# Kernel tuning notes

Measured on AMD Instinct MI355X. Metric: run time of the kernel, lower is better.

Reference implementation:

```python
import jax, jax.numpy as jnp
import numpy as np
from itertools import product

_N = 50000
_G = 52  # voxel grid extent


def _build_maps():
    rs = np.random.RandomState(0)
    ids = rs.choice(_G ** 3, size=_N, replace=False)
    coords = np.stack(np.unravel_index(ids, (_G, _G, _G)), axis=1)  # [N,3]
    order = np.argsort(ids)
    sorted_ids = ids[order]
    in_lists, out_lists = [], []
    for off in product((-1, 0, 1), repeat=3):
        nb = coords + np.array(off)
        valid = np.all((nb >= 0) & (nb < _G), axis=1)
        nb_id = nb[:, 0] * _G * _G + nb[:, 1] * _G + nb[:, 2]
        pos = np.searchsorted(sorted_ids, nb_id)
        pos_c = np.minimum(pos, _N - 1)
        found = valid & (sorted_ids[pos_c] == nb_id)
        in_lists.append(order[pos_c[found]].astype(np.int32))
        out_lists.append(np.nonzero(found)[0].astype(np.int32))
    P = max(len(a) for a in in_lists)  # identity offset -> P == N
    K = len(in_lists)
    in_idx = np.full((K, P), _N, dtype=np.int32)   # sentinel = zero row
    out_idx = np.full((K, P), _N, dtype=np.int32)  # sentinel = dummy out row
    for k in range(K):
        in_idx[k, : len(in_lists[k])] = in_lists[k]
        out_idx[k, : len(out_lists[k])] = out_lists[k]
    pid = (coords[:, 0] // 2) * 26 * 26 + (coords[:, 1] // 2) * 26 + (coords[:, 2] // 2)
    uniq, inv = np.unique(pid, return_inverse=True)
    return in_idx, out_idx, inv.astype(np.int32), int(len(uniq))


def setup_inputs() -> dict:
    key = jax.random.key(0)
    ks = jax.random.split(key, 10)
    in_idx, out_idx, pool_idx, num_pool = _build_maps()
    s1 = 1.0 / np.sqrt(27 * 256)
    s2 = 1.0 / np.sqrt(27 * 512)
    return {
        "feats": jax.random.normal(ks[0], (_N, 256), jnp.float32),
        "W1": jax.random.normal(ks[1], (27, 256, 512), jnp.float32) * s1,
        "g1": 1.0 + 0.1 * jax.random.normal(ks[2], (512,), jnp.float32),
        "b1": 0.05 * jax.random.normal(ks[3], (512,), jnp.float32),
        "W2": jax.random.normal(ks[4], (27, 512, 512), jnp.float32) * s2,
        "g2": 1.0 + 0.1 * jax.random.normal(ks[5], (512,), jnp.float32),
        "b2": 0.05 * jax.random.normal(ks[6], (512,), jnp.float32),
        "W3": jax.random.normal(ks[7], (27, 512, 512), jnp.float32) * s2,
        "g3": 1.0 + 0.1 * jax.random.normal(ks[8], (512,), jnp.float32),
        "b3": 0.05 * jax.random.normal(ks[9], (512,), jnp.float32),
        "in_idx": jnp.asarray(in_idx),
        "out_idx": jnp.asarray(out_idx),
        "pool_idx": jnp.asarray(pool_idx),
        "num_pool": num_pool,
    }


def _sparse_conv(feats, W, in_idx, out_idx):
    # gather-GEMM-scatter over K=27 kernel offsets (MinkowskiConvolution)
    N, Cin = feats.shape
    fp = jnp.concatenate([feats, jnp.zeros((1, Cin), feats.dtype)], axis=0)
    acc0 = jnp.zeros((N + 1, W.shape[-1]), feats.dtype)  # last row = dummy sink
    def step(acc, xs):
        ii, oi, Wk = xs
        return acc.at[oi].add(fp[ii] @ Wk), None
    acc, _ = jax.lax.scan(step, acc0, (in_idx, out_idx, W))
    return acc[:N]


def _bn_relu(x, g, b, eps=1e-5):
    m = x.mean(axis=0)
    v = x.var(axis=0)  # biased, matching torch BN normalization
    return jax.nn.relu((x - m) * jax.lax.rsqrt(v + eps) * g + b)


def reference(feats, W1, g1, b1, W2, g2, b2, W3, g3, b3, in_idx, out_idx, pool_idx, num_pool):
    x = _bn_relu(_sparse_conv(feats, W1, in_idx, out_idx), g1, b1)
    x = _bn_relu(_sparse_conv(x, W2, in_idx, out_idx), g2, b2)
    x = _bn_relu(_sparse_conv(x, W3, in_idx, out_idx), g3, b3)
    return jax.ops.segment_max(x, pool_idx, num_segments=num_pool)
```

## Files before the change

### kernel.cpp

```cpp
#include <hip/hip_runtime.h>
#include <hip/hip_bf16.h>
#include <stdint.h>

typedef __attribute__((ext_vector_type(8))) short bf16x8;
typedef __attribute__((ext_vector_type(4))) float f32x4;
typedef unsigned short u16;

__device__ __forceinline__ u16 f2bf(float x) {
  unsigned u = __float_as_uint(x);
  unsigned r = (u + 0x7FFFu + ((u >> 16) & 1u)) >> 16;
  return (u16)r;
}

__device__ __forceinline__ void gl_lds16(const void* g, void* l) {
  __builtin_amdgcn_global_load_lds((const __attribute__((address_space(1))) void*)g,
                                   (__attribute__((address_space(3))) void*)l, 16, 0, 0);
}


__global__ void zero_i32_kernel(int* p, int n) {
  int i = blockIdx.x * blockDim.x + threadIdx.x;
  if (i < n) p[i] = 0;
}

__global__ void init_nbr_kernel(int* nbr, int total, int N) {
  for (int i = blockIdx.x * blockDim.x + threadIdx.x; i < total; i += gridDim.x * blockDim.x)
    nbr[i] = N;
}

__global__ void scatter_nbr_kernel(const int* __restrict__ in_idx, const int* __restrict__ out_idx,
                                   int* __restrict__ nbr, int N, int P, int NPAD) {
  const int total = 27 * P;
  for (int i = blockIdx.x * blockDim.x + threadIdx.x; i < total; i += gridDim.x * blockDim.x) {
    const int o = out_idx[i];
    if ((unsigned)o < (unsigned)N) {
      const int k = i / P;
      nbr[(size_t)k * NPAD + o] = in_idx[i];
    }
  }
}

__global__ void cvt_feats_kernel(const float* __restrict__ F, u16* __restrict__ X0, int N) {
  const int total = (N + 1) * 64;
  for (int i = blockIdx.x * blockDim.x + threadIdx.x; i < total; i += gridDim.x * blockDim.x) {
    const int r = i >> 6;
    ushort4 o;
    if (r < N) {
      const float4 v = ((const float4*)F)[i];
      o.x = f2bf(v.x); o.y = f2bf(v.y); o.z = f2bf(v.z); o.w = f2bf(v.w);
    } else {
      o.x = 0; o.y = 0; o.z = 0; o.w = 0;
    }
    ((ushort4*)X0)[i] = o;
  }
}

__global__ void cvt_w_kernel(const float* __restrict__ W, u16* __restrict__ Wt, int CIN) {
  __shared__ float t[32][33];
  const int k = blockIdx.z;
  const int c0 = blockIdx.y * 32;
  const int n0 = blockIdx.x * 32;
  const int tx = threadIdx.x, ty = threadIdx.y;
  const float* Wk = W + (size_t)k * CIN * 512;
  for (int i = ty; i < 32; i += 8)
    t[i][tx] = Wk[(size_t)(c0 + i) * 512 + n0 + tx];
  __syncthreads();
  u16* Wtk = Wt + (size_t)k * 512 * CIN;
  for (int i = ty; i < 32; i += 8)
    Wtk[(size_t)(n0 + i) * CIN + c0 + tx] = f2bf(t[tx][i]);
}


__global__ void scatter_members_kernel(const int* __restrict__ pool_idx, int* __restrict__ gcnt,
                                       int* __restrict__ mlist, int N) {
  const int r = blockIdx.x * blockDim.x + threadIdx.x;
  if (r < N) {
    const int p = pool_idx[r];
    const int pos = atomicAdd(&gcnt[p], 1);
    if (pos < 8) mlist[p * 8 + pos] = r;
  }
}

__global__ void pool_grouped_kernel(const float* __restrict__ Y, const float* __restrict__ sc,
                                    const float* __restrict__ sh, const int* __restrict__ gcnt,
                                    const int* __restrict__ mlist, float* __restrict__ out) {
  const int p = blockIdx.x;
  const int t = threadIdx.x;
  const int c = t * 2;
  const float s0 = sc[c], s1 = sc[c + 1];
  const float h0 = sh[c], h1 = sh[c + 1];
  int n = gcnt[p];
  if (n > 8) n = 8;
  float m0 = 0.f, m1 = 0.f;
  for (int i = 0; i < n; ++i) {
    const int r = mlist[p * 8 + i];
    const float2 v = *(const float2*)&Y[(size_t)r * 512 + c];
    m0 = fmaxf(m0, fmaxf(fmaf(v.x, s0, h0), 0.f));
    m1 = fmaxf(m1, fmaxf(fmaf(v.y, s1, h1), 0.f));
  }
  float2 o; o.x = m0; o.y = m1;
  *(float2*)&out[(size_t)p * 512 + c] = o;
}


template <int CIN>
__global__ __launch_bounds__(256, 2) void conv_kernel(
    const u16* __restrict__ X,
    const u16* __restrict__ Wt,
    const int* __restrict__ nbr,
    float* __restrict__ Y,
    float* __restrict__ st,
    int N, int NPAD) {
  constexpr int KK = CIN / 32;
  constexpr int NSTEPS = 27 * KK;
  __shared__ __align__(16) u16 lds[16384];

  const int tid = threadIdx.x;
  const int lane = tid & 63;
  const int wv = tid >> 6;
  const int wm = wv >> 1, wn = wv & 1;

  int bid = blockIdx.x;
  if ((gridDim.x & 7) == 0) {
    const int cpx = gridDim.x >> 3;
    bid = (bid & 7) * cpx + (bid >> 3);
  }
  const int row0 = (bid >> 2) * 128;
  const int col0 = (bid & 3) * 128;

  const int sc = tid & 3;
  int srow[2], scs[2];
  size_t boffg[2];
#pragma unroll
  for (int i = 0; i < 2; ++i) {
    srow[i] = i * 64 + (tid >> 2);
    scs[i] = (sc ^ ((srow[i] >> 1) & 3)) * 8;
    boffg[i] = (size_t)(col0 + srow[i]) * CIN + scs[i];
  }

  const int lr = lane & 15;
  const int q = lane >> 4;
  int aoff[4], boff[4];
#pragma unroll
  for (int f = 0; f < 4; ++f) {
    const int ra = wm * 64 + f * 16 + lr;
    aoff[f] = ra * 32 + ((q ^ ((ra >> 1) & 3)) * 8);
    const int rb = wn * 64 + f * 16 + lr;
    boff[f] = 4096 + rb * 32 + ((q ^ ((rb >> 1) & 3)) * 8);
  }

  f32x4 acc[4][4];
#pragma unroll
  for (int a = 0; a < 4; ++a)
#pragma unroll
    for (int b = 0; b < 4; ++b) acc[a][b] = (f32x4){0.f, 0.f, 0.f, 0.f};

  size_t arow[2];
#pragma unroll
  for (int i = 0; i < 2; ++i) arow[i] = (size_t)nbr[row0 + srow[i]] * CIN;

#pragma unroll
  for (int i = 0; i < 2; ++i) {
    gl_lds16(X + arow[i] + scs[i], &lds[i * 2048 + wv * 512]);
    gl_lds16(Wt + boffg[i], &lds[4096 + i * 2048 + wv * 512]);
  }

  int cur = 0;
  for (int s = 0; s < NSTEPS; ++s) {
    __syncthreads();
    const int ns = s + 1;
    if (ns < NSTEPS) {
      const int k = ns / KK;
      const int kk = ns % KK;
      if (kk == 0) {
        const int* nb = nbr + (size_t)k * NPAD + row0;
#pragma unroll
        for (int i = 0; i < 2; ++i) arow[i] = (size_t)nb[srow[i]] * CIN;
      }
      const int nxt = cur ^ 1;
      const int ko = kk * 32;
      const size_t kb = (size_t)k * (512 * CIN);
#pragma unroll
      for (int i = 0; i < 2; ++i) {
        gl_lds16(X + arow[i] + ko + scs[i], &lds[nxt * 8192 + i * 2048 + wv * 512]);
        gl_lds16(Wt + kb + boffg[i] + ko, &lds[nxt * 8192 + 4096 + i * 2048 + wv * 512]);
      }
    }
    const u16* lb = &lds[cur * 8192];
    bf16x8 av[4], bv[4];
#pragma unroll
    for (int f = 0; f < 4; ++f) av[f] = *(const bf16x8*)&lb[aoff[f]];
#pragma unroll
    for (int f = 0; f < 4; ++f) bv[f] = *(const bf16x8*)&lb[boff[f]];
#pragma unroll
    for (int a = 0; a < 4; ++a)
#pragma unroll
      for (int b = 0; b < 4; ++b)
        acc[a][b] = __builtin_amdgcn_mfma_f32_16x16x32_bf16(av[a], bv[b], acc[a][b], 0, 0, 0);
    cur ^= 1;
  }

#pragma unroll
  for (int a = 0; a < 4; ++a) {
    const int r0 = row0 + wm * 64 + a * 16 + q * 4;
#pragma unroll
    for (int b = 0; b < 4; ++b) {
      const int c = col0 + wn * 64 + b * 16 + lr;
#pragma unroll
      for (int j = 0; j < 4; ++j) {
        const int r = r0 + j;
        if (r < N) Y[(size_t)r * 512 + c] = acc[a][b][j];
      }
    }
  }

  __syncthreads();
  float* fls = (float*)lds;
  if (tid < 256) fls[tid] = 0.f;
  __syncthreads();
#pragma unroll
  for (int b = 0; b < 4; ++b) {
    float s = 0.f, q2 = 0.f;
#pragma unroll
    for (int a = 0; a < 4; ++a) {
      const int rbase = row0 + wm * 64 + a * 16 + q * 4;
#pragma unroll
      for (int j = 0; j < 4; ++j) {
        if (rbase + j < N) {
          const float v = acc[a][b][j];
          s += v; q2 += v * v;
        }
      }
    }
    s += __shfl_xor(s, 16);  s += __shfl_xor(s, 32);
    q2 += __shfl_xor(q2, 16); q2 += __shfl_xor(q2, 32);
    if (q == 0) {
      const int cl = wn * 64 + b * 16 + lr;
      atomicAdd(&fls[cl], s);
      atomicAdd(&fls[128 + cl], q2);
    }
  }
  __syncthreads();
  if (tid < 128) {
    atomicAdd(&st[col0 + tid], fls[tid]);
    atomicAdd(&st[512 + col0 + tid], fls[128 + tid]);
  }
}


__global__ void bn_finalize_kernel(const float* __restrict__ st, const float* __restrict__ g,
                                   const float* __restrict__ b, float* __restrict__ sc,
                                   float* __restrict__ sh, int N) {
  const int c = threadIdx.x;
  if (c < 512) {
    const float inv = 1.f / (float)N;
    const float m = st[c] * inv;
    const float v = st[512 + c] * inv - m * m;
    const float rs = rsqrtf(v + 1e-5f);
    const float s = rs * g[c];
    sc[c] = s;
    sh[c] = b[c] - m * s;
  }
}

__global__ void bn_norm_kernel(const float* __restrict__ Y, const float* __restrict__ sc,
                               const float* __restrict__ sh, u16* __restrict__ Xn, int N) {
  const int total = (N + 1) * 128;
  for (int i = blockIdx.x * blockDim.x + threadIdx.x; i < total; i += gridDim.x * blockDim.x) {
    const int r = i >> 7;
    const int c = (i & 127) * 4;
    ushort4 o;
    if (r < N) {
      const float4 y = *(const float4*)&Y[(size_t)r * 512 + c];
      const float v0 = fmaxf(fmaf(y.x, sc[c + 0], sh[c + 0]), 0.f);
      const float v1 = fmaxf(fmaf(y.y, sc[c + 1], sh[c + 1]), 0.f);
      const float v2 = fmaxf(fmaf(y.z, sc[c + 2], sh[c + 2]), 0.f);
      const float v3 = fmaxf(fmaf(y.w, sc[c + 3], sh[c + 3]), 0.f);
      o.x = f2bf(v0); o.y = f2bf(v1); o.z = f2bf(v2); o.w = f2bf(v3);
    } else {
      o.x = 0; o.y = 0; o.z = 0; o.w = 0;
    }
    *(ushort4*)&Xn[(size_t)r * 512 + c] = o;
  }
}


extern "C" void kernel_launch(void* const* d_in, const int* in_sizes, int n_in,
                              void* d_out, int out_size, void* d_ws, size_t ws_size,
                              hipStream_t stream) {
  const float* feats = (const float*)d_in[0];
  const float* W1 = (const float*)d_in[1];
  const float* g1 = (const float*)d_in[2];
  const float* b1 = (const float*)d_in[3];
  const float* W2 = (const float*)d_in[4];
  const float* g2 = (const float*)d_in[5];
  const float* b2 = (const float*)d_in[6];
  const float* W3 = (const float*)d_in[7];
  const float* g3 = (const float*)d_in[8];
  const float* b3 = (const float*)d_in[9];
  const int* in_idx = (const int*)d_in[10];
  const int* out_idx = (const int*)d_in[11];
  const int* pool_idx = (const int*)d_in[12];
  float* out = (float*)d_out;

  const int N = in_sizes[0] / 256;
  const int P = in_sizes[10] / 27;
  const int NPAD = ((N + 127) / 128) * 128;
  const int npool = out_size / 512;
  (void)n_in; (void)ws_size;

  char* w = (char*)d_ws;
  size_t off = 0;
  auto carve = [&](size_t bytes) {
    void* p = w + off;
    off += (bytes + 511) & ~(size_t)511;
    return p;
  };
  u16* X0 = (u16*)carve((size_t)(N + 1) * 256 * 2);
  u16* X1 = (u16*)carve((size_t)(N + 1) * 512 * 2);
  float* Y = (float*)carve((size_t)N * 512 * 4);
  u16* W1t = (u16*)carve((size_t)27 * 512 * 256 * 2);
  u16* W2t = (u16*)carve((size_t)27 * 512 * 512 * 2);
  u16* W3t = (u16*)carve((size_t)27 * 512 * 512 * 2);
  float* st0 = (float*)carve(1024 * 4);
  float* st1 = (float*)carve(1024 * 4);
  float* st2 = (float*)carve(1024 * 4);
  float* sc = (float*)carve(512 * 4);
  float* sh = (float*)carve(512 * 4);
  int* nbr = (int*)carve((size_t)27 * NPAD * 4);

  int* gcnt = (int*)X0;
  int* mlist = (int*)((char*)X0 + (1 << 17));

  const int convGrid = (NPAD / 128) * 4;

  zero_i32_kernel<<<4, 256, 0, stream>>>((int*)st0, 1024);
  zero_i32_kernel<<<4, 256, 0, stream>>>((int*)st1, 1024);
  zero_i32_kernel<<<4, 256, 0, stream>>>((int*)st2, 1024);
  init_nbr_kernel<<<2048, 256, 0, stream>>>(nbr, 27 * NPAD, N);
  scatter_nbr_kernel<<<2048, 256, 0, stream>>>(in_idx, out_idx, nbr, N, P, NPAD);
  cvt_feats_kernel<<<2048, 256, 0, stream>>>(feats, X0, N);
  cvt_w_kernel<<<dim3(16, 8, 27), dim3(32, 8), 0, stream>>>(W1, W1t, 256);
  cvt_w_kernel<<<dim3(16, 16, 27), dim3(32, 8), 0, stream>>>(W2, W2t, 512);
  cvt_w_kernel<<<dim3(16, 16, 27), dim3(32, 8), 0, stream>>>(W3, W3t, 512);

  conv_kernel<256><<<convGrid, 256, 0, stream>>>(X0, W1t, nbr, Y, st0, N, NPAD);
  zero_i32_kernel<<<(npool + 255) / 256, 256, 0, stream>>>(gcnt, npool);
  scatter_members_kernel<<<(N + 255) / 256, 256, 0, stream>>>(pool_idx, gcnt, mlist, N);
  bn_finalize_kernel<<<1, 512, 0, stream>>>(st0, g1, b1, sc, sh, N);
  bn_norm_kernel<<<4096, 256, 0, stream>>>(Y, sc, sh, X1, N);

  conv_kernel<512><<<convGrid, 256, 0, stream>>>(X1, W2t, nbr, Y, st1, N, NPAD);
  bn_finalize_kernel<<<1, 512, 0, stream>>>(st1, g2, b2, sc, sh, N);
  bn_norm_kernel<<<4096, 256, 0, stream>>>(Y, sc, sh, X1, N);

  conv_kernel<512><<<convGrid, 256, 0, stream>>>(X1, W3t, nbr, Y, st2, N, NPAD);
  bn_finalize_kernel<<<1, 512, 0, stream>>>(st2, g3, b3, sc, sh, N);
  pool_grouped_kernel<<<npool, 256, 0, stream>>>(Y, sc, sh, gcnt, mlist, out);
}
```

Measured before the change: 1.807 ms.

## Triple-buffer conv mainloop with explicit vmcnt waits and early neighbor-index prefetch

Replaces the double-buffered gather-GEMM loop with a three-slot LDS ring that keeps two stages of global-to-LDS loads in flight. Each step waits with an explicit s_waitcnt vmcnt and a raw barrier instead of __syncthreads. The neighbor indices for the next kernel offset are fetched two sub-steps ahead, so gather address computation no longer stalls at offset boundaries. The MFMA block is also wrapped in s_setprio. LDS use per block grows from 32KB to 48KB, and correctness now depends on hand-counted vmcnt values matching the number of outstanding loads.

Measured after the change: 1.778 ms. About the same (-1.6%).

```diff
diff --git a/kernel.cpp b/kernel.cpp
--- a/kernel.cpp
+++ b/kernel.cpp
@@ -112,8 +112,7 @@
     float* __restrict__ st,
     int N, int NPAD) {
   constexpr int KK = CIN / 32;
-  constexpr int NSTEPS = 27 * KK;
-  __shared__ __align__(16) u16 lds[16384];
+  __shared__ __align__(16) u16 lds[24576];
 
   const int tid = threadIdx.x;
   const int lane = tid & 63;
@@ -128,15 +127,10 @@
   const int row0 = (bid >> 2) * 128;
   const int col0 = (bid & 3) * 128;
 
-  const int sc = tid & 3;
-  int srow[2], scs[2];
-  size_t boffg[2];
-#pragma unroll
-  for (int i = 0; i < 2; ++i) {
-    srow[i] = i * 64 + (tid >> 2);
-    scs[i] = (sc ^ ((srow[i] >> 1) & 3)) * 8;
-    boffg[i] = (size_t)(col0 + srow[i]) * CIN + scs[i];
-  }
+  const int srow = tid >> 2;
+  const int scs = (((tid & 3) ^ ((srow >> 1) & 3)) * 8);
+  const size_t boffg0 = (size_t)(col0 + srow) * CIN + scs;
+  const size_t boffg1 = (size_t)(col0 + 64 + srow) * CIN + scs;
 
   const int lr = lane & 15;
   const int q = lane >> 4;
@@ -155,50 +149,76 @@
 #pragma unroll
     for (int b = 0; b < 4; ++b) acc[a][b] = (f32x4){0.f, 0.f, 0.f, 0.f};
 
-  size_t arow[2];
-#pragma unroll
-  for (int i = 0; i < 2; ++i) arow[i] = (size_t)nbr[row0 + srow[i]] * CIN;
-
-#pragma unroll
-  for (int i = 0; i < 2; ++i) {
-    gl_lds16(X + arow[i] + scs[i], &lds[i * 2048 + wv * 512]);
-    gl_lds16(Wt + boffg[i], &lds[4096 + i * 2048 + wv * 512]);
-  }
-
-  int cur = 0;
-  for (int s = 0; s < NSTEPS; ++s) {
-    __syncthreads();
-    const int ns = s + 1;
-    if (ns < NSTEPS) {
-      const int k = ns / KK;
-      const int kk = ns % KK;
-      if (kk == 0) {
-        const int* nb = nbr + (size_t)k * NPAD + row0;
-#pragma unroll
-        for (int i = 0; i < 2; ++i) arow[i] = (size_t)nb[srow[i]] * CIN;
+  auto stage = [&](int slot, size_t a0, size_t a1, int ko, size_t kb) {
+    u16* sb = &lds[slot * 8192];
+    gl_lds16(X + a0 + ko + scs, &sb[wv * 512]);
+    gl_lds16(X + a1 + ko + scs, &sb[2048 + wv * 512]);
+    gl_lds16(Wt + kb + boffg0 + ko, &sb[4096 + wv * 512]);
+    gl_lds16(Wt + kb + boffg1 + ko, &sb[6144 + wv * 512]);
+  };
+
+  size_t arow0 = (size_t)nbr[row0 + srow] * CIN;
+  size_t arow1 = (size_t)nbr[row0 + 64 + srow] * CIN;
+  stage(0, arow0, arow1, 0, 0);
+  stage(1, arow0, arow1, 32, 0);
+
+  int sl = 0, sl2 = 2;
+  int nn0 = 0, nn1 = 0;
+
+#define STEP_BODY(WAITN, DO_NBR, DO_STAGE, A0, A1, KO, KB)                        \
+  {                                                                               \
+    asm volatile("s_waitcnt vmcnt(" #WAITN ")" ::: "memory");                     \
+    __builtin_amdgcn_s_barrier();                                                 \
+    asm volatile("" ::: "memory");                                                \
+    const u16* lb = &lds[sl * 8192];                                              \
+    bf16x8 av[4], bv[4];                                                          \
+    _Pragma("unroll") for (int f = 0; f < 4; ++f) av[f] = *(const bf16x8*)&lb[aoff[f]]; \
+    _Pragma("unroll") for (int f = 0; f < 4; ++f) bv[f] = *(const bf16x8*)&lb[boff[f]]; \
+    __builtin_amdgcn_sched_barrier(0);                                            \
+    if (DO_NBR) {                                                                 \
+      nn0 = nbr[(size_t)(s + 1) * NPAD + row0 + srow];                            \
+      nn1 = nbr[(size_t)(s + 1) * NPAD + row0 + 64 + srow];                       \
+    }                                                                             \
+    if (DO_STAGE) stage(sl2, (A0), (A1), (KO), (KB));                             \
+    __builtin_amdgcn_sched_barrier(0);                                            \
+    __builtin_amdgcn_s_setprio(1);                                                \
+    _Pragma("unroll") for (int a = 0; a < 4; ++a)                                 \
+      _Pragma("unroll") for (int b = 0; b < 4; ++b)                               \
+        acc[a][b] = __builtin_amdgcn_mfma_f32_16x16x32_bf16(av[a], bv[b], acc[a][b], 0, 0, 0); \
+    __builtin_amdgcn_s_setprio(0);                                                \
+    sl = (sl == 2) ? 0 : sl + 1;                                                  \
+    sl2 = (sl2 == 2) ? 0 : sl2 + 1;                                               \
+  }
+
+  for (int s = 0; s < 26; ++s) {
+    const size_t kbC = (size_t)s * (512 * CIN);
+    const size_t kbN = (size_t)(s + 1) * (512 * CIN);
+#pragma unroll
+    for (int kk = 0; kk < KK; ++kk) {
+      const bool donbr = (kk == 2);
+      if (kk < KK - 2) {
+        if (kk == 3) STEP_BODY(6, donbr, true, arow0, arow1, (kk + 2) * 32, kbC)
+        else         STEP_BODY(4, donbr, true, arow0, arow1, (kk + 2) * 32, kbC)
+      } else {
+        STEP_BODY(4, false, true, (size_t)nn0 * CIN, (size_t)nn1 * CIN,
+                  (kk + 2 - KK) * 32, kbN)
       }
-      const int nxt = cur ^ 1;
-      const int ko = kk * 32;
-      const size_t kb = (size_t)k * (512 * CIN);
-#pragma unroll
-      for (int i = 0; i < 2; ++i) {
-        gl_lds16(X + arow[i] + ko + scs[i], &lds[nxt * 8192 + i * 2048 + wv * 512]);
-        gl_lds16(Wt + kb + boffg[i] + ko, &lds[nxt * 8192 + 4096 + i * 2048 + wv * 512]);
-      }
-    }
-    const u16* lb = &lds[cur * 8192];
-    bf16x8 av[4], bv[4];
-#pragma unroll
-    for (int f = 0; f < 4; ++f) av[f] = *(const bf16x8*)&lb[aoff[f]];
-#pragma unroll
-    for (int f = 0; f < 4; ++f) bv[f] = *(const bf16x8*)&lb[boff[f]];
-#pragma unroll
-    for (int a = 0; a < 4; ++a)
-#pragma unroll
-      for (int b = 0; b < 4; ++b)
-        acc[a][b] = __builtin_amdgcn_mfma_f32_16x16x32_bf16(av[a], bv[b], acc[a][b], 0, 0, 0);
-    cur ^= 1;
-  }
+    }
+    arow0 = (size_t)nn0 * CIN;
+    arow1 = (size_t)nn1 * CIN;
+  }
+  {
+    const int s = 26;
+    const size_t kbC = (size_t)s * (512 * CIN);
+    (void)s;
+#pragma unroll
+    for (int kk = 0; kk < KK; ++kk) {
+      if (kk < KK - 2)      STEP_BODY(4, false, true, arow0, arow1, (kk + 2) * 32, kbC)
+      else if (kk < KK - 1) STEP_BODY(4, false, false, arow0, arow1, 0, kbC)
+      else                  STEP_BODY(0, false, false, arow0, arow1, 0, kbC)
+    }
+  }
+#undef STEP_BODY
 
 #pragma unroll
   for (int a = 0; a < 4; ++a) {
```

## Load conv weight fragments directly to registers, halve LDS, raise occupancy

Applied to the files above, without the earlier changes.

The B (weight) operand no longer goes through LDS. Each wave loads its MFMA fragments straight from global memory into registers, and the next step's fragments are prefetched. LDS then holds only the gathered A rows, so the buffer is halved and launch bounds ask for 3 blocks per SM. The cost is that the two wn-waves each fetch the same weight bytes uncoalesced from global/L2, and more registers are needed for the prefetched fragments.

After: 3.993 ms. 2.21x slower.

```diff
diff --git a/kernel.cpp b/kernel.cpp
--- a/kernel.cpp
+++ b/kernel.cpp
@@ -104,7 +104,7 @@
 
 
 template <int CIN>
-__global__ __launch_bounds__(256, 2) void conv_kernel(
+__global__ __launch_bounds__(256, 3) void conv_kernel(
     const u16* __restrict__ X,
     const u16* __restrict__ Wt,
     const int* __restrict__ nbr,
@@ -113,7 +113,7 @@
     int N, int NPAD) {
   constexpr int KK = CIN / 32;
   constexpr int NSTEPS = 27 * KK;
-  __shared__ __align__(16) u16 lds[16384];
+  __shared__ __align__(16) u16 lds[8192];
 
   const int tid = threadIdx.x;
   const int lane = tid & 63;
@@ -128,26 +128,21 @@
   const int row0 = (bid >> 2) * 128;
   const int col0 = (bid & 3) * 128;
 
-  const int sc = tid & 3;
-  int srow[2], scs[2];
-  size_t boffg[2];
-#pragma unroll
-  for (int i = 0; i < 2; ++i) {
-    srow[i] = i * 64 + (tid >> 2);
-    scs[i] = (sc ^ ((srow[i] >> 1) & 3)) * 8;
-    boffg[i] = (size_t)(col0 + srow[i]) * CIN + scs[i];
-  }
+  const int srow = tid >> 2;
+  const int scs = (((tid & 3) ^ ((srow >> 1) & 3)) * 8);
 
   const int lr = lane & 15;
   const int q = lane >> 4;
-  int aoff[4], boff[4];
+  int aoff[4];
 #pragma unroll
   for (int f = 0; f < 4; ++f) {
     const int ra = wm * 64 + f * 16 + lr;
     aoff[f] = ra * 32 + ((q ^ ((ra >> 1) & 3)) * 8);
-    const int rb = wn * 64 + f * 16 + lr;
-    boff[f] = 4096 + rb * 32 + ((q ^ ((rb >> 1) & 3)) * 8);
-  }
+  }
+  size_t bfrag[4];
+#pragma unroll
+  for (int f = 0; f < 4; ++f)
+    bfrag[f] = (size_t)(col0 + wn * 64 + f * 16 + lr) * CIN + q * 8;
 
   f32x4 acc[4][4];
 #pragma unroll
@@ -155,15 +150,14 @@
 #pragma unroll
     for (int b = 0; b < 4; ++b) acc[a][b] = (f32x4){0.f, 0.f, 0.f, 0.f};
 
-  size_t arow[2];
-#pragma unroll
-  for (int i = 0; i < 2; ++i) arow[i] = (size_t)nbr[row0 + srow[i]] * CIN;
-
-#pragma unroll
-  for (int i = 0; i < 2; ++i) {
-    gl_lds16(X + arow[i] + scs[i], &lds[i * 2048 + wv * 512]);
-    gl_lds16(Wt + boffg[i], &lds[4096 + i * 2048 + wv * 512]);
-  }
+  size_t arow0 = (size_t)nbr[row0 + srow] * CIN;
+  size_t arow1 = (size_t)nbr[row0 + 64 + srow] * CIN;
+
+  gl_lds16(X + arow0 + scs, &lds[wv * 512]);
+  gl_lds16(X + arow1 + scs, &lds[2048 + wv * 512]);
+  bf16x8 bvC[4], bvN[4];
+#pragma unroll
+  for (int f = 0; f < 4; ++f) bvC[f] = *(const bf16x8*)(Wt + bfrag[f]);
 
   int cur = 0;
   for (int s = 0; s < NSTEPS; ++s) {
@@ -174,29 +168,31 @@
       const int kk = ns % KK;
       if (kk == 0) {
         const int* nb = nbr + (size_t)k * NPAD + row0;
-#pragma unroll
-        for (int i = 0; i < 2; ++i) arow[i] = (size_t)nb[srow[i]] * CIN;
+        arow0 = (size_t)nb[srow] * CIN;
+        arow1 = (size_t)nb[64 + srow] * CIN;
       }
       const int nxt = cur ^ 1;
       const int ko = kk * 32;
       const size_t kb = (size_t)k * (512 * CIN);
-#pragma unroll
-      for (int i = 0; i < 2; ++i) {
-        gl_lds16(X + arow[i] + ko + scs[i], &lds[nxt * 8192 + i * 2048 + wv * 512]);
-        gl_lds16(Wt + kb + boffg[i] + ko, &lds[nxt * 8192 + 4096 + i * 2048 + wv * 512]);
-      }
-    }
-    const u16* lb = &lds[cur * 8192];
-    bf16x8 av[4], bv[4];
+      gl_lds16(X + arow0 + ko + scs, &lds[nxt * 4096 + wv * 512]);
+      gl_lds16(X + arow1 + ko + scs, &lds[nxt * 4096 + 2048 + wv * 512]);
+      const u16* bp = Wt + kb + ko;
+#pragma unroll
+      for (int f = 0; f < 4; ++f) bvN[f] = *(const bf16x8*)(bp + bfrag[f]);
+    }
+    __builtin_amdgcn_sched_barrier(0);
+
+    const u16* lb = &lds[cur * 4096];
+    bf16x8 av[4];
 #pragma unroll
     for (int f = 0; f < 4; ++f) av[f] = *(const bf16x8*)&lb[aoff[f]];
 #pragma unroll
-    for (int f = 0; f < 4; ++f) bv[f] = *(const bf16x8*)&lb[boff[f]];
-#pragma unroll
     for (int a = 0; a < 4; ++a)
 #pragma unroll
       for (int b = 0; b < 4; ++b)
-        acc[a][b] = __builtin_amdgcn_mfma_f32_16x16x32_bf16(av[a], bv[b], acc[a][b], 0, 0, 0);
+        acc[a][b] = __builtin_amdgcn_mfma_f32_16x16x32_bf16(av[a], bvC[b], acc[a][b], 0, 0, 0);
+#pragma unroll
+    for (int f = 0; f < 4; ++f) bvC[f] = bvN[f];
     cur ^= 1;
   }
 
```
